# Kernel tuning notes

Hardware: AMD Instinct MI355X
Metric: run time of the kernel (lower is better)

The kernel has to match this reference:

```python
import jax, jax.numpy as jnp
import numpy as np

B, U, F = 32768, 256, 256  # batch, units, input features
LR = 0.01                  # inner_lr
EPS = 1e-3                 # TF LayerNormalization default epsilon


def _layer_norm(x, gamma, beta):
    m = jnp.mean(x, axis=-1, keepdims=True)
    v = jnp.var(x, axis=-1, keepdims=True)
    return (x - m) * jax.lax.rsqrt(v + EPS) * gamma + beta


def _enc(W1, b1, W2, b2, u):
    # mlp_2 inner encoder: Dense(4U, gelu-exact) -> Dense(U)
    return jax.nn.gelu(u @ W1 + b1, approximate=False) @ W2 + b2


def setup_inputs() -> dict:
    key = jax.random.key(0)
    ks = jax.random.split(key, 12)
    def w(k, shape):
        fan_in = shape[0]
        return jax.random.normal(k, shape, jnp.float32) / np.sqrt(fan_in)
    return {
        "x": jax.random.normal(ks[0], (B, F), jnp.float32),
        "h_prev": jax.random.normal(ks[1], (B, U), jnp.float32),
        "W_phi": w(ks[2], (F + U, U)), "b_phi": jnp.zeros((U,), jnp.float32),
        "W_psi": w(ks[3], (F + U, U)), "b_psi": jnp.zeros((U,), jnp.float32),
        "W1": w(ks[4], (U, 4 * U)), "b1": jnp.zeros((4 * U,), jnp.float32),
        "W2": w(ks[5], (4 * U, U)), "b2": jnp.zeros((U,), jnp.float32),
        "W_g": w(ks[6], (U, U)), "g_bias": jnp.zeros((U,), jnp.float32),
        "ln_gamma": jnp.ones((U,), jnp.float32), "ln_beta": jnp.zeros((U,), jnp.float32),
        "W_h": w(ks[7], (U, U)), "h_bias": jnp.zeros((U,), jnp.float32),
    }


def reference(x, h_prev, W_phi, b_phi, W_psi, b_psi, W1, b1, W2, b2,
              W_g, g_bias, ln_gamma, ln_beta, W_h, h_bias):
    z = jnp.concatenate([x, h_prev], axis=-1)          # [B, F+U]
    phi = z @ W_phi + b_phi                            # [B, U], also the inner target

    def inner_loss(params):
        W1_, b1_, W2_, b2_ = params
        r = _enc(W1_, b1_, W2_, b2_, phi) @ W_g + g_bias
        r = _layer_norm(r, ln_gamma, ln_beta)
        return jnp.mean(jnp.square(r - phi)), r

    params = (W1, b1, W2, b2)
    # inner_iterations = 1: one SGD step on the inner-encoder weights only
    (_, recon), grads = jax.value_and_grad(inner_loss, has_aux=True)(params)
    params = tuple(p - LR * g for p, g in zip(params, grads))

    psi = z @ W_psi + b_psi                            # [B, U]
    feat = _enc(*params, psi) + 0.1 * recon            # updated encoder on psi
    out = feat @ W_h + h_bias                          # new hidden / cell output
    return out
```

## Files before the change

kernel.cpp:

```cpp
#include <hip/hip_runtime.h>
#include <math.h>

#define B_N 32768
#define U_N 256
#define H_N 1024
#define LR_C 0.01f
#define EPS_C 1e-3f

typedef unsigned short ushort_t;
typedef unsigned int uint_t;
using frag8 = __attribute__((ext_vector_type(8))) short;
using f32x4 = __attribute__((ext_vector_type(4))) float;

__device__ __forceinline__ float erf_fast(float y) {
    float ay = fabsf(y);
    float t = __builtin_amdgcn_rcpf(fmaf(0.3275911f, ay, 1.0f));
    float p = fmaf(1.061405429f, t, -1.453152027f);
    p = fmaf(p, t, 1.421413741f);
    p = fmaf(p, t, -0.284496736f);
    p = fmaf(p, t, 0.254829592f);
    p = p * t;
    float e = __expf(-ay * ay);
    float r = fmaf(-p, e, 1.0f);
    return copysignf(r, y);
}
__device__ __forceinline__ float gelu_f(float x) {
    return 0.5f * x * (1.0f + erf_fast(x * 0.7071067811865475f));
}
__device__ __forceinline__ float dgelu_f(float x) {
    float c = 0.5f * (1.0f + erf_fast(x * 0.7071067811865475f));
    float p = 0.3989422804014327f * __expf(-0.5f * x * x);
    return fmaf(x, p, c);
}
__device__ __forceinline__ void splitf(float v, ushort_t& h, ushort_t& l) {
    uint_t u = __float_as_uint(v);
    h = (ushort_t)(u >> 16);
    float r = v - __uint_as_float(u & 0xFFFF0000u);
    uint_t ru = __float_as_uint(r);
    l = (ushort_t)((ru + 0x7FFFu + ((ru >> 16) & 1u)) >> 16);
}
__device__ __forceinline__ ushort_t cvt_rne(float v) {
    uint_t u = __float_as_uint(v);
    return (ushort_t)((u + 0x7FFFu + ((u >> 16) & 1u)) >> 16);
}
__device__ __forceinline__ float bf2f(ushort_t u) {
    return __uint_as_float((uint_t)u << 16);
}
__device__ __forceinline__ void unpack2(uint_t pa, uint_t pb, uint_t& hw, uint_t& lw) {
    hw = __builtin_amdgcn_perm(pb, pa, 0x07060302u);
    lw = __builtin_amdgcn_perm(pb, pa, 0x05040100u);
}

#define EPI_NONE 0
#define EPI_GELU 1
#define EPI_ADDS 3

#define BEP_P   0
#define BEP_PT  1
#define BEP_A1  2
#define BEP_DAT 3

template<int ACONCAT, int APACK, int EPI, int OPACK>
__global__ __launch_bounds__(256)
void mgemm_k(const float* A, const float* A2, const uint_t* __restrict__ AP,
             const ushort_t* __restrict__ BTh, const ushort_t* __restrict__ BTl,
             const float* __restrict__ bias, const ushort_t* __restrict__ Xr,
             float* C, uint_t* Cp,
             int M, int N, int K)
{
    __shared__ ushort_t Ah[128 * 40], Al[128 * 40];
    __shared__ ushort_t Bh[128 * 40], Bl[128 * 40];
    const int tid = threadIdx.x;
    const int m0 = blockIdx.x * 128, n0 = blockIdx.y * 128;
    const int lane = tid & 63, w = tid >> 6;
    const int wm = (w & 1) * 64, wn = (w >> 1) * 64;
    const int fr = lane & 15, fq = lane >> 4;
    const int sr = tid >> 1;
    const int sk = (tid & 1) * 16;

    f32x4 acc[4][4];
    #pragma unroll
    for (int i = 0; i < 4; i++)
        #pragma unroll
        for (int j = 0; j < 4; j++) acc[i][j] = (f32x4){0.f, 0.f, 0.f, 0.f};

    for (int k0 = 0; k0 < K; k0 += 32) {
        if (APACK) {
            const uint_t* ap = AP + (size_t)(m0 + sr) * K + k0 + sk;
            uint4 p0 = *(const uint4*)(ap);
            uint4 p1 = *(const uint4*)(ap + 4);
            uint4 p2 = *(const uint4*)(ap + 8);
            uint4 p3 = *(const uint4*)(ap + 12);
            uint4 h0, h1, l0, l1;
            unpack2(p0.x, p0.y, h0.x, l0.x); unpack2(p0.z, p0.w, h0.y, l0.y);
            unpack2(p1.x, p1.y, h0.z, l0.z); unpack2(p1.z, p1.w, h0.w, l0.w);
            unpack2(p2.x, p2.y, h1.x, l1.x); unpack2(p2.z, p2.w, h1.y, l1.y);
            unpack2(p3.x, p3.y, h1.z, l1.z); unpack2(p3.z, p3.w, h1.w, l1.w);
            *(uint4*)&Ah[sr * 40 + sk]     = h0;
            *(uint4*)&Ah[sr * 40 + sk + 8] = h1;
            *(uint4*)&Al[sr * 40 + sk]     = l0;
            *(uint4*)&Al[sr * 40 + sk + 8] = l1;
        } else {
            #pragma unroll
            for (int g = 0; g < 2; g++) {
                uint4 qh, qa;
                uint_t ph[4], pl[4];
                #pragma unroll
                for (int c = 0; c < 2; c++) {
                    const int ak = k0 + sk + g * 8 + c * 4;
                    const float* ap;
                    if (ACONCAT) ap = (ak < 256) ? (A + (size_t)(m0 + sr) * 256 + ak)
                                                 : (A2 + (size_t)(m0 + sr) * 256 + (ak - 256));
                    else         ap = A + (size_t)(m0 + sr) * K + ak;
                    float4 v = *(const float4*)ap;
                    ushort_t h0,h1,h2,h3,l0,l1,l2,l3;
                    splitf(v.x,h0,l0); splitf(v.y,h1,l1); splitf(v.z,h2,l2); splitf(v.w,h3,l3);
                    ph[c*2]   = (uint_t)h0 | ((uint_t)h1 << 16);
                    ph[c*2+1] = (uint_t)h2 | ((uint_t)h3 << 16);
                    pl[c*2]   = (uint_t)l0 | ((uint_t)l1 << 16);
                    pl[c*2+1] = (uint_t)l2 | ((uint_t)l3 << 16);
                }
                qh.x = ph[0]; qh.y = ph[1]; qh.z = ph[2]; qh.w = ph[3];
                qa.x = pl[0]; qa.y = pl[1]; qa.z = pl[2]; qa.w = pl[3];
                *(uint4*)&Ah[sr * 40 + sk + g * 8] = qh;
                *(uint4*)&Al[sr * 40 + sk + g * 8] = qa;
            }
        }
        {
            const size_t bo = (size_t)(n0 + sr) * K + k0 + sk;
            *(uint4*)&Bh[sr * 40 + sk]     = *(const uint4*)&BTh[bo];
            *(uint4*)&Bh[sr * 40 + sk + 8] = *(const uint4*)&BTh[bo + 8];
            *(uint4*)&Bl[sr * 40 + sk]     = *(const uint4*)&BTl[bo];
            *(uint4*)&Bl[sr * 40 + sk + 8] = *(const uint4*)&BTl[bo + 8];
        }
        __syncthreads();

        frag8 afh[4], afl[4], bfh[4], bfl[4];
        #pragma unroll
        for (int i = 0; i < 4; i++) {
            const int ar = wm + i * 16 + fr;
            afh[i] = *(frag8*)&Ah[ar * 40 + fq * 8];
            afl[i] = *(frag8*)&Al[ar * 40 + fq * 8];
        }
        #pragma unroll
        for (int j = 0; j < 4; j++) {
            const int br = wn + j * 16 + fr;
            bfh[j] = *(frag8*)&Bh[br * 40 + fq * 8];
            bfl[j] = *(frag8*)&Bl[br * 40 + fq * 8];
        }
        #pragma unroll
        for (int i = 0; i < 4; i++)
            #pragma unroll
            for (int j = 0; j < 4; j++) {
                acc[i][j] = __builtin_amdgcn_mfma_f32_16x16x32_bf16(afh[i], bfh[j], acc[i][j], 0, 0, 0);
                acc[i][j] = __builtin_amdgcn_mfma_f32_16x16x32_bf16(afh[i], bfl[j], acc[i][j], 0, 0, 0);
                acc[i][j] = __builtin_amdgcn_mfma_f32_16x16x32_bf16(afl[i], bfh[j], acc[i][j], 0, 0, 0);
            }
        __syncthreads();
    }

    float bv[4] = {0.f, 0.f, 0.f, 0.f};
    if (bias != nullptr)
        #pragma unroll
        for (int j = 0; j < 4; j++) bv[j] = bias[n0 + wn + j * 16 + fr];
    #pragma unroll
    for (int i = 0; i < 4; i++)
        #pragma unroll
        for (int j = 0; j < 4; j++) {
            const int col = n0 + wn + j * 16 + fr;
            #pragma unroll
            for (int r = 0; r < 4; r++) {
                const int row = m0 + wm + i * 16 + fq * 4 + r;
                const size_t off = (size_t)row * N + col;
                float c = acc[i][j][r] + bv[j];
                if (EPI == EPI_GELU)      c = gelu_f(c);
                else if (EPI == EPI_ADDS) c = c + 0.1f * bf2f(Xr[off]);
                if (OPACK) {
                    ushort_t h, l;
                    splitf(c, h, l);
                    Cp[off] = ((uint_t)h << 16) | (uint_t)l;
                } else {
                    C[off] = c;
                }
            }
        }
}

template<int ACONCAT, int BEP>
__global__ __launch_bounds__(256)
void bgemm_k(const void* Av, const float* A2f, const ushort_t* __restrict__ BTh,
             const float* __restrict__ bias, const ushort_t* __restrict__ GpIn,
             ushort_t* Crm, ushort_t* Cct, ushort_t* GpOut,
             int M, int N, int K)
{
    __shared__ ushort_t Ah[128 * 40];
    __shared__ ushort_t Bh[128 * 40];
    const int tid = threadIdx.x;
    const int m0 = blockIdx.x * 128, n0 = blockIdx.y * 128;
    const int lane = tid & 63, w = tid >> 6;
    const int wm = (w & 1) * 64, wn = (w >> 1) * 64;
    const int fr = lane & 15, fq = lane >> 4;
    const int sr = tid >> 1;
    const int sk = (tid & 1) * 16;

    f32x4 acc[4][4];
    #pragma unroll
    for (int i = 0; i < 4; i++)
        #pragma unroll
        for (int j = 0; j < 4; j++) acc[i][j] = (f32x4){0.f, 0.f, 0.f, 0.f};

    for (int k0 = 0; k0 < K; k0 += 32) {
        if (ACONCAT) {
            const float* A = (const float*)Av;
            #pragma unroll
            for (int g = 0; g < 2; g++) {
                uint_t ph[4];
                #pragma unroll
                for (int c = 0; c < 2; c++) {
                    const int ak = k0 + sk + g * 8 + c * 4;
                    const float* ap = (ak < 256) ? (A + (size_t)(m0 + sr) * 256 + ak)
                                                 : (A2f + (size_t)(m0 + sr) * 256 + (ak - 256));
                    float4 v = *(const float4*)ap;
                    ph[c*2]   = (uint_t)cvt_rne(v.x) | ((uint_t)cvt_rne(v.y) << 16);
                    ph[c*2+1] = (uint_t)cvt_rne(v.z) | ((uint_t)cvt_rne(v.w) << 16);
                }
                uint4 q; q.x = ph[0]; q.y = ph[1]; q.z = ph[2]; q.w = ph[3];
                *(uint4*)&Ah[sr * 40 + sk + g * 8] = q;
            }
        } else {
            const ushort_t* A = (const ushort_t*)Av;
            const size_t ao = (size_t)(m0 + sr) * K + k0 + sk;
            *(uint4*)&Ah[sr * 40 + sk]     = *(const uint4*)&A[ao];
            *(uint4*)&Ah[sr * 40 + sk + 8] = *(const uint4*)&A[ao + 8];
        }
        {
            const size_t bo = (size_t)(n0 + sr) * K + k0 + sk;
            *(uint4*)&Bh[sr * 40 + sk]     = *(const uint4*)&BTh[bo];
            *(uint4*)&Bh[sr * 40 + sk + 8] = *(const uint4*)&BTh[bo + 8];
        }
        __syncthreads();

        frag8 af[4], bf[4];
        #pragma unroll
        for (int i = 0; i < 4; i++) af[i] = *(frag8*)&Ah[(wm + i * 16 + fr) * 40 + fq * 8];
        #pragma unroll
        for (int j = 0; j < 4; j++) bf[j] = *(frag8*)&Bh[(wn + j * 16 + fr) * 40 + fq * 8];
        #pragma unroll
        for (int i = 0; i < 4; i++)
            #pragma unroll
            for (int j = 0; j < 4; j++)
                acc[i][j] = __builtin_amdgcn_mfma_f32_16x16x32_bf16(af[i], bf[j], acc[i][j], 0, 0, 0);
        __syncthreads();
    }

    float bv[4] = {0.f, 0.f, 0.f, 0.f};
    if (bias != nullptr)
        #pragma unroll
        for (int j = 0; j < 4; j++) bv[j] = bias[n0 + wn + j * 16 + fr];
    #pragma unroll
    for (int i = 0; i < 4; i++)
        #pragma unroll
        for (int j = 0; j < 4; j++) {
            const int col = n0 + wn + j * 16 + fr;
            const int rowb = m0 + wm + i * 16 + fq * 4;
            float v[4];
            #pragma unroll
            for (int r = 0; r < 4; r++) v[r] = acc[i][j][r] + bv[j];
            if (BEP == BEP_A1) {
                ushort_t gc[4];
                #pragma unroll
                for (int r = 0; r < 4; r++) {
                    float g = gelu_f(v[r]);
                    gc[r] = cvt_rne(g);
                    Crm[(size_t)(rowb + r) * N + col] = gc[r];
                    GpOut[(size_t)(rowb + r) * N + col] = cvt_rne(dgelu_f(v[r]));
                }
                uint_t p0 = (uint_t)gc[0] | ((uint_t)gc[1] << 16);
                uint_t p1 = (uint_t)gc[2] | ((uint_t)gc[3] << 16);
                *(uint2*)&Cct[(size_t)col * M + rowb] = (uint2){p0, p1};
            } else if (BEP == BEP_DAT) {
                ushort_t dc[4];
                #pragma unroll
                for (int r = 0; r < 4; r++)
                    dc[r] = cvt_rne(v[r] * bf2f(GpIn[(size_t)(rowb + r) * N + col]));
                uint_t p0 = (uint_t)dc[0] | ((uint_t)dc[1] << 16);
                uint_t p1 = (uint_t)dc[2] | ((uint_t)dc[3] << 16);
                *(uint2*)&Cct[(size_t)col * M + rowb] = (uint2){p0, p1};
            } else {
                ushort_t cc[4];
                #pragma unroll
                for (int r = 0; r < 4; r++) {
                    cc[r] = cvt_rne(v[r]);
                    Crm[(size_t)(rowb + r) * N + col] = cc[r];
                }
                if (BEP == BEP_PT) {
                    uint_t p0 = (uint_t)cc[0] | ((uint_t)cc[1] << 16);
                    uint_t p1 = (uint_t)cc[2] | ((uint_t)cc[3] << 16);
                    *(uint2*)&Cct[(size_t)col * M + rowb] = (uint2){p0, p1};
                }
            }
        }
}

__global__ __launch_bounds__(256)
void wgrad_k(const ushort_t* __restrict__ AT, const ushort_t* __restrict__ BTt,
             float* C, int M, int N, int KA, int kofsA, int KB, int kofsB, int KC)
{
    __shared__ ushort_t Ah[128 * 40];
    __shared__ ushort_t Bh[128 * 40];
    const int tid = threadIdx.x;
    const int m0 = blockIdx.x * 128, n0 = blockIdx.y * 128;
    const int kbA = kofsA + blockIdx.z * KC;
    const int kbB = kofsB + blockIdx.z * KC;
    const int lane = tid & 63, w = tid >> 6;
    const int wm = (w & 1) * 64, wn = (w >> 1) * 64;
    const int fr = lane & 15, fq = lane >> 4;
    const int sr = tid >> 1;
    const int sk = (tid & 1) * 16;

    f32x4 acc[4][4];
    #pragma unroll
    for (int i = 0; i < 4; i++)
        #pragma unroll
        for (int j = 0; j < 4; j++) acc[i][j] = (f32x4){0.f, 0.f, 0.f, 0.f};

    for (int k0 = 0; k0 < KC; k0 += 32) {
        const size_t ao = (size_t)(m0 + sr) * KA + kbA + k0 + sk;
        *(uint4*)&Ah[sr * 40 + sk]     = *(const uint4*)&AT[ao];
        *(uint4*)&Ah[sr * 40 + sk + 8] = *(const uint4*)&AT[ao + 8];
        const size_t bo = (size_t)(n0 + sr) * KB + kbB + k0 + sk;
        *(uint4*)&Bh[sr * 40 + sk]     = *(const uint4*)&BTt[bo];
        *(uint4*)&Bh[sr * 40 + sk + 8] = *(const uint4*)&BTt[bo + 8];
        __syncthreads();

        frag8 af[4], bf[4];
        #pragma unroll
        for (int i = 0; i < 4; i++) af[i] = *(frag8*)&Ah[(wm + i * 16 + fr) * 40 + fq * 8];
        #pragma unroll
        for (int j = 0; j < 4; j++) bf[j] = *(frag8*)&Bh[(wn + j * 16 + fr) * 40 + fq * 8];
        #pragma unroll
        for (int i = 0; i < 4; i++)
            #pragma unroll
            for (int j = 0; j < 4; j++)
                acc[i][j] = __builtin_amdgcn_mfma_f32_16x16x32_bf16(af[i], bf[j], acc[i][j], 0, 0, 0);
        __syncthreads();
    }
    #pragma unroll
    for (int i = 0; i < 4; i++)
        #pragma unroll
        for (int j = 0; j < 4; j++) {
            const int col = n0 + wn + j * 16 + fr;
            #pragma unroll
            for (int r = 0; r < 4; r++) {
                const int row = m0 + wm + i * 16 + fq * 4 + r;
                atomicAdd(&C[(size_t)row * N + col], acc[i][j][r]);
            }
        }
}

__global__ __launch_bounds__(256)
void colsumT_k(const ushort_t* __restrict__ T, float* db, int LD, int cols)
{
    const int n = blockIdx.x * 4 + (threadIdx.x >> 6);
    const int lane = threadIdx.x & 63;
    const ushort_t* row = T + (size_t)n * LD;
    float s = 0.f;
    for (int c = lane * 8; c < cols; c += 512) {
        uint4 q = *(const uint4*)&row[c];
        uint_t u[4] = {q.x, q.y, q.z, q.w};
        #pragma unroll
        for (int t = 0; t < 4; t++) {
            s += bf2f((ushort_t)(u[t] & 0xFFFF));
            s += bf2f((ushort_t)(u[t] >> 16));
        }
    }
    #pragma unroll
    for (int o = 32; o > 0; o >>= 1) s += __shfl_xor(s, o);
    if (lane == 0) atomicAdd(&db[n], s);
}

__global__ __launch_bounds__(256)
void ln_bf_k(const ushort_t* r0, const ushort_t* __restrict__ phi,
             const float* __restrict__ gamma, const float* __restrict__ beta,
             ushort_t* recon, ushort_t* dr0)
{
    const int lane = threadIdx.x & 63;
    const int wv = threadIdx.x >> 6;
    const int row = blockIdx.x * 4 + wv;
    const size_t base = (size_t)row * U_N + (lane << 2);

    uint2 xu = *(const uint2*)(r0 + base);
    uint2 pu = *(const uint2*)(phi + base);
    float xs[4] = { bf2f((ushort_t)(xu.x & 0xFFFF)), bf2f((ushort_t)(xu.x >> 16)),
                    bf2f((ushort_t)(xu.y & 0xFFFF)), bf2f((ushort_t)(xu.y >> 16)) };
    float ps[4] = { bf2f((ushort_t)(pu.x & 0xFFFF)), bf2f((ushort_t)(pu.x >> 16)),
                    bf2f((ushort_t)(pu.y & 0xFFFF)), bf2f((ushort_t)(pu.y >> 16)) };
    float s = xs[0] + xs[1] + xs[2] + xs[3];
    float sq = xs[0]*xs[0] + xs[1]*xs[1] + xs[2]*xs[2] + xs[3]*xs[3];
    #pragma unroll
    for (int o = 32; o > 0; o >>= 1) { s += __shfl_xor(s, o); sq += __shfl_xor(sq, o); }
    const float m   = s * (1.0f / U_N);
    const float var = sq * (1.0f / U_N) - m * m;
    const float inv = rsqrtf(var + EPS_C);

    float4 gv = *(const float4*)(gamma + (lane << 2));
    float4 bvv = *(const float4*)(beta + (lane << 2));
    float gs[4] = {gv.x, gv.y, gv.z, gv.w};
    float bs[4] = {bvv.x, bvv.y, bvv.z, bvv.w};
    float rh[4], dh[4], rc[4];
    float s1 = 0.f, s2 = 0.f;
    const float gscale = 2.0f / ((float)B_N * (float)U_N);
    #pragma unroll
    for (int j = 0; j < 4; j++) {
        rh[j] = (xs[j] - m) * inv;
        rc[j] = rh[j] * gs[j] + bs[j];
        float g2 = gscale * (rc[j] - ps[j]);
        dh[j] = g2 * gs[j];
        s1 += dh[j];
        s2 += dh[j] * rh[j];
    }
    #pragma unroll
    for (int o = 32; o > 0; o >>= 1) { s1 += __shfl_xor(s1, o); s2 += __shfl_xor(s2, o); }
    const float mu1 = s1 * (1.0f / U_N);
    const float mu2 = s2 * (1.0f / U_N);
    ushort_t oc[4], dc[4];
    #pragma unroll
    for (int j = 0; j < 4; j++) {
        oc[j] = cvt_rne(rc[j]);
        dc[j] = cvt_rne(inv * (dh[j] - mu1 - rh[j] * mu2));
    }
    *(uint2*)(recon + base) = (uint2){ (uint_t)oc[0] | ((uint_t)oc[1] << 16),
                                       (uint_t)oc[2] | ((uint_t)oc[3] << 16) };
    *(uint2*)(dr0 + base)   = (uint2){ (uint_t)dc[0] | ((uint_t)dc[1] << 16),
                                       (uint_t)dc[2] | ((uint_t)dc[3] << 16) };
}

template<int HASL>
__global__ __launch_bounds__(256)
void tsplit_k(const float* __restrict__ W, ushort_t* __restrict__ Th,
              ushort_t* __restrict__ Tl, int R, int C)
{
    __shared__ float t[64][65];
    const int tid = threadIdx.x;
    const int R0 = blockIdx.x * 64, C0 = blockIdx.y * 64;
    const int c = tid & 63, rb = (tid >> 6) * 16;
    for (int i = 0; i < 16; i++)
        t[rb + i][c] = W[(size_t)(R0 + rb + i) * C + C0 + c];
    __syncthreads();
    const int orr = tid & 63, ob = (tid >> 6) * 16;
    for (int i = 0; i < 16; i++) {
        const int oc = ob + i;
        ushort_t h, l;
        splitf(t[orr][oc], h, l);
        Th[(size_t)(C0 + oc) * R + R0 + orr] = h;
        if (HASL) Tl[(size_t)(C0 + oc) * R + R0 + orr] = l;
    }
}

__global__ __launch_bounds__(256)
void tupd_k(const float* __restrict__ W, const float* __restrict__ dW,
            ushort_t* __restrict__ Th, ushort_t* __restrict__ Tl, int R, int C)
{
    __shared__ float t[64][65];
    const int tid = threadIdx.x;
    const int R0 = blockIdx.x * 64, C0 = blockIdx.y * 64;
    const int c = tid & 63, rb = (tid >> 6) * 16;
    for (int i = 0; i < 16; i++) {
        const size_t o = (size_t)(R0 + rb + i) * C + C0 + c;
        t[rb + i][c] = W[o] - LR_C * dW[o];
    }
    __syncthreads();
    const int orr = tid & 63, ob = (tid >> 6) * 16;
    for (int i = 0; i < 16; i++) {
        const int oc = ob + i;
        ushort_t h, l;
        splitf(t[orr][oc], h, l);
        Th[(size_t)(C0 + oc) * R + R0 + orr] = h;
        Tl[(size_t)(C0 + oc) * R + R0 + orr] = l;
    }
}

__global__ __launch_bounds__(256)
void scvt_k(const float* __restrict__ W, ushort_t* __restrict__ Th, int n4)
{
    const int i = blockIdx.x * 256 + threadIdx.x;
    if (i >= n4) return;
    float4 v = *(const float4*)(W + (size_t)i * 4);
    uint2 ph;
    ph.x = (uint_t)cvt_rne(v.x) | ((uint_t)cvt_rne(v.y) << 16);
    ph.y = (uint_t)cvt_rne(v.z) | ((uint_t)cvt_rne(v.w) << 16);
    *(uint2*)&Th[(size_t)i * 4] = ph;
}

__global__ __launch_bounds__(256)
void bupd_k(const float* __restrict__ b1, const float* __restrict__ db1,
            const float* __restrict__ b2, const float* __restrict__ db2,
            float* __restrict__ b1u, float* __restrict__ b2u)
{
    const int i = blockIdx.x * 256 + threadIdx.x;
    if (i < H_N) b1u[i] = b1[i] - LR_C * db1[i];
    else if (i < H_N + U_N) b2u[i - H_N] = b2[i - H_N] - LR_C * db2[i - H_N];
}

extern "C" void kernel_launch(void* const* d_in, const int* in_sizes, int n_in,
                              void* d_out, int out_size, void* d_ws, size_t ws_size,
                              hipStream_t stream)
{
    const float* x      = (const float*)d_in[0];
    const float* h_prev = (const float*)d_in[1];
    const float* W_phi  = (const float*)d_in[2];
    const float* b_phi  = (const float*)d_in[3];
    const float* W_psi  = (const float*)d_in[4];
    const float* b_psi  = (const float*)d_in[5];
    const float* W1     = (const float*)d_in[6];
    const float* b1     = (const float*)d_in[7];
    const float* W2     = (const float*)d_in[8];
    const float* b2     = (const float*)d_in[9];
    const float* W_g    = (const float*)d_in[10];
    const float* g_bias = (const float*)d_in[11];
    const float* gamma  = (const float*)d_in[12];
    const float* beta   = (const float*)d_in[13];
    const float* W_h    = (const float*)d_in[14];
    const float* h_bias = (const float*)d_in[15];
    float* out = (float*)d_out;

    const size_t BU = (size_t)B_N * U_N;
    const size_t UH = (size_t)U_N * H_N;

    float* ws  = (float*)d_ws;
    float* dW1 = ws;
    float* db1 = dW1 + UH;
    float* dW2 = db1 + H_N;
    float* db2 = dW2 + UH;
    float* b1u = db2 + U_N;
    float* b2u = b1u + H_N;
    ushort_t* us = (ushort_t*)(((uintptr_t)(b2u + U_N) + 15) & ~(uintptr_t)15);
    ushort_t* WphiT_h = us;
    ushort_t* WpsiT_h = WphiT_h + 131072;     ushort_t* WpsiT_l = WpsiT_h + 131072;
    ushort_t* W1T_h   = WpsiT_l + 131072;
    ushort_t* W2T_h   = W1T_h + 262144;
    ushort_t* W2s_h   = W2T_h + 262144;
    ushort_t* Wgs_h   = W2s_h + 262144;
    ushort_t* WgT_h   = Wgs_h + 65536;
    ushort_t* W1uT_h  = WgT_h + 65536;        ushort_t* W1uT_l = W1uT_h + 262144;
    ushort_t* W2uT_h  = W1uT_l + 262144;      ushort_t* W2uT_l = W2uT_h + 262144;
    ushort_t* WhT_h   = W2uT_l + 262144;      ushort_t* WhT_l  = WhT_h + 65536;
    ushort_t* phi_bf  = WhT_l + 65536;
    ushort_t* phiT_bf = phi_bf + BU;
    ushort_t* recon_bf= phiT_bf + BU;
    ushort_t* chunk0  = recon_bf + BU;
    const size_t P_bytes = (size_t)((char*)chunk0 - (char*)d_ws);

    int GA = 2;
    while (GA < 256 && P_bytes + (size_t)(B_N / GA) * 10240 + (1 << 20) > ws_size) GA *= 2;
    size_t region = (size_t)(B_N / GA) * 10240;
    int GC = 1;
    while (GC < 256) {
        size_t cC = (size_t)(B_N / GC) * 6144;
        size_t r = cC > region ? cC : region;
        if (P_bytes + r + (1 << 20) <= ws_size) { region = r; break; }
        GC *= 2;
    }
    const int BcA = B_N / GA;
    const int BcC = B_N / GC;
    const int KC = (BcA >= 8192) ? 512 : ((BcA >= 1024) ? BcA / 16 : BcA);
    const int Z  = BcA / KC;

    ushort_t* g1  = chunk0;
    ushort_t* gp  = g1  + (size_t)BcA * H_N;
    ushort_t* g1T = gp  + (size_t)BcA * H_N;
    ushort_t* daT = g1T + (size_t)BcA * H_N;
    ushort_t* e_b = daT + (size_t)BcA * H_N;
    ushort_t* r0b = e_b + (size_t)BcA * U_N;
    ushort_t* deb = r0b + (size_t)BcA * U_N;
    ushort_t* deT = deb + (size_t)BcA * U_N;
    uint_t* psi_p  = (uint_t*)chunk0;
    uint_t* h2_p   = psi_p + (size_t)BcC * U_N;
    uint_t* feat_p = h2_p  + (size_t)BcC * H_N;

    hipMemsetAsync(dW1, 0, (2 * UH + H_N + U_N) * sizeof(float), stream);

    dim3 blk(256);
    tsplit_k<0><<<dim3(8, 4),  blk, 0, stream>>>(W_phi, WphiT_h, nullptr, 512, 256);
    tsplit_k<1><<<dim3(8, 4),  blk, 0, stream>>>(W_psi, WpsiT_h, WpsiT_l, 512, 256);
    tsplit_k<0><<<dim3(4, 16), blk, 0, stream>>>(W1, W1T_h, nullptr, 256, 1024);
    tsplit_k<0><<<dim3(16, 4), blk, 0, stream>>>(W2, W2T_h, nullptr, 1024, 256);
    tsplit_k<0><<<dim3(4, 4),  blk, 0, stream>>>(W_g, WgT_h, nullptr, 256, 256);
    tsplit_k<1><<<dim3(4, 4),  blk, 0, stream>>>(W_h, WhT_h, WhT_l, 256, 256);
    scvt_k<<<dim3(256), blk, 0, stream>>>(W2, W2s_h, 65536);
    scvt_k<<<dim3(64),  blk, 0, stream>>>(W_g, Wgs_h, 16384);

    bgemm_k<1, BEP_PT><<<dim3(B_N / 128, 2), blk, 0, stream>>>(
        x, h_prev, WphiT_h, b_phi, nullptr, phi_bf, phiT_bf, nullptr, B_N, U_N, 512);

    for (int c = 0; c < GA; c++) {
        const size_t off = (size_t)c * BcA;
        const ushort_t* phic = phi_bf + off * U_N;
        bgemm_k<0, BEP_A1><<<dim3(BcA / 128, 8), blk, 0, stream>>>(
            phic, nullptr, W1T_h, b1, nullptr, g1, g1T, gp, BcA, H_N, U_N);
        bgemm_k<0, BEP_P><<<dim3(BcA / 128, 2), blk, 0, stream>>>(
            g1, nullptr, W2T_h, b2, nullptr, e_b, nullptr, nullptr, BcA, U_N, H_N);
        bgemm_k<0, BEP_P><<<dim3(BcA / 128, 2), blk, 0, stream>>>(
            e_b, nullptr, WgT_h, g_bias, nullptr, r0b, nullptr, nullptr, BcA, U_N, U_N);
        ln_bf_k<<<dim3(BcA / 4), blk, 0, stream>>>(r0b, phic, gamma, beta,
                                                   recon_bf + off * U_N, r0b);
        bgemm_k<0, BEP_PT><<<dim3(BcA / 128, 2), blk, 0, stream>>>(
            r0b, nullptr, Wgs_h, nullptr, nullptr, deb, deT, nullptr, BcA, U_N, U_N);
        bgemm_k<0, BEP_DAT><<<dim3(BcA / 128, 8), blk, 0, stream>>>(
            deb, nullptr, W2s_h, nullptr, gp, nullptr, daT, nullptr, BcA, H_N, U_N);
        wgrad_k<<<dim3(8, 2, Z), blk, 0, stream>>>(g1T, deT, dW2, H_N, U_N,
                                                   BcA, 0, BcA, 0, KC);
        colsumT_k<<<dim3(U_N / 4), blk, 0, stream>>>(deT, db2, BcA, BcA);
        wgrad_k<<<dim3(2, 8, Z), blk, 0, stream>>>(phiT_bf, daT, dW1, U_N, H_N,
                                                   B_N, (int)off, BcA, 0, KC);
        colsumT_k<<<dim3(H_N / 4), blk, 0, stream>>>(daT, db1, BcA, BcA);
    }

    bupd_k<<<dim3(5), blk, 0, stream>>>(b1, db1, b2, db2, b1u, b2u);
    tupd_k<<<dim3(4, 16), blk, 0, stream>>>(W1, dW1, W1uT_h, W1uT_l, 256, 1024);
    tupd_k<<<dim3(16, 4), blk, 0, stream>>>(W2, dW2, W2uT_h, W2uT_l, 1024, 256);

    for (int c = 0; c < GC; c++) {
        const size_t off = (size_t)c * BcC;
        mgemm_k<1, 0, EPI_NONE, 1><<<dim3(BcC / 128, 2), blk, 0, stream>>>(
            x + off * 256, h_prev + off * U_N, nullptr,
            WpsiT_h, WpsiT_l, b_psi, nullptr,
            nullptr, psi_p, BcC, U_N, 512);
        mgemm_k<0, 1, EPI_GELU, 1><<<dim3(BcC / 128, 8), blk, 0, stream>>>(
            nullptr, nullptr, psi_p,
            W1uT_h, W1uT_l, b1u, nullptr,
            nullptr, h2_p, BcC, H_N, U_N);
        mgemm_k<0, 1, EPI_ADDS, 1><<<dim3(BcC / 128, 2), blk, 0, stream>>>(
            nullptr, nullptr, h2_p,
            W2uT_h, W2uT_l, b2u, recon_bf + off * U_N,
            nullptr, feat_p, BcC, U_N, H_N);
        mgemm_k<0, 1, EPI_NONE, 0><<<dim3(BcC / 128, 2), blk, 0, stream>>>(
            nullptr, nullptr, feat_p,
            WhT_h, WhT_l, h_bias, nullptr,
            out + off * U_N, nullptr, BcC, U_N, U_N);
    }
}
```

Before: 876.7 us.

## Double-buffer LDS tiles with register prefetch and swap grid axes for N-major order

All three GEMM kernels now prefetch the next K-tile from global memory into registers while the MFMA loop runs on the current tile. The prefetched tile is then written into a second LDS buffer, so only one barrier is needed per iteration and load latency is hidden behind compute. The launch grids are also transposed so the N tiles vary fastest, letting neighbouring blocks share the same A rows in cache. The cost is double the LDS (80 KB dynamic for the split kernel) and more registers, which can lower occupancy.

```diff
diff --git a/kernel.cpp b/kernel.cpp
--- a/kernel.cpp
+++ b/kernel.cpp
@@ -68,10 +68,13 @@
              float* C, uint_t* Cp,
              int M, int N, int K)
 {
-    __shared__ ushort_t Ah[128 * 40], Al[128 * 40];
-    __shared__ ushort_t Bh[128 * 40], Bl[128 * 40];
+    extern __shared__ ushort_t smem[];
+    ushort_t* AhS = smem;
+    ushort_t* AlS = smem + 10240;
+    ushort_t* BhS = smem + 20480;
+    ushort_t* BlS = smem + 30720;
     const int tid = threadIdx.x;
-    const int m0 = blockIdx.x * 128, n0 = blockIdx.y * 128;
+    const int m0 = blockIdx.y * 128, n0 = blockIdx.x * 128;
     const int lane = tid & 63, w = tid >> 6;
     const int wm = (w & 1) * 64, wn = (w >> 1) * 64;
     const int fr = lane & 15, fq = lane >> 4;
@@ -84,57 +87,84 @@
         #pragma unroll
         for (int j = 0; j < 4; j++) acc[i][j] = (f32x4){0.f, 0.f, 0.f, 0.f};
 
-    for (int k0 = 0; k0 < K; k0 += 32) {
+    uint4 rA[4];
+    float4 rF[4];
+    uint4 rB[4];
+
+    auto load_tile = [&](int k0) {
         if (APACK) {
             const uint_t* ap = AP + (size_t)(m0 + sr) * K + k0 + sk;
-            uint4 p0 = *(const uint4*)(ap);
-            uint4 p1 = *(const uint4*)(ap + 4);
-            uint4 p2 = *(const uint4*)(ap + 8);
-            uint4 p3 = *(const uint4*)(ap + 12);
+            rA[0] = *(const uint4*)(ap);
+            rA[1] = *(const uint4*)(ap + 4);
+            rA[2] = *(const uint4*)(ap + 8);
+            rA[3] = *(const uint4*)(ap + 12);
+        } else {
+            #pragma unroll
+            for (int g = 0; g < 4; g++) {
+                const int ak = k0 + sk + g * 4;
+                const float* ap;
+                if (ACONCAT) ap = (ak < 256) ? (A + (size_t)(m0 + sr) * 256 + ak)
+                                             : (A2 + (size_t)(m0 + sr) * 256 + (ak - 256));
+                else         ap = A + (size_t)(m0 + sr) * K + ak;
+                rF[g] = *(const float4*)ap;
+            }
+        }
+        const size_t bo = (size_t)(n0 + sr) * K + k0 + sk;
+        rB[0] = *(const uint4*)&BTh[bo];
+        rB[1] = *(const uint4*)&BTh[bo + 8];
+        rB[2] = *(const uint4*)&BTl[bo];
+        rB[3] = *(const uint4*)&BTl[bo + 8];
+    };
+    auto store_tile = [&](int buf) {
+        ushort_t* Ah = AhS + buf * 5120;
+        ushort_t* Al = AlS + buf * 5120;
+        ushort_t* Bh = BhS + buf * 5120;
+        ushort_t* Bl = BlS + buf * 5120;
+        if (APACK) {
             uint4 h0, h1, l0, l1;
-            unpack2(p0.x, p0.y, h0.x, l0.x); unpack2(p0.z, p0.w, h0.y, l0.y);
-            unpack2(p1.x, p1.y, h0.z, l0.z); unpack2(p1.z, p1.w, h0.w, l0.w);
-            unpack2(p2.x, p2.y, h1.x, l1.x); unpack2(p2.z, p2.w, h1.y, l1.y);
-            unpack2(p3.x, p3.y, h1.z, l1.z); unpack2(p3.z, p3.w, h1.w, l1.w);
+            unpack2(rA[0].x, rA[0].y, h0.x, l0.x); unpack2(rA[0].z, rA[0].w, h0.y, l0.y);
+            unpack2(rA[1].x, rA[1].y, h0.z, l0.z); unpack2(rA[1].z, rA[1].w, h0.w, l0.w);
+            unpack2(rA[2].x, rA[2].y, h1.x, l1.x); unpack2(rA[2].z, rA[2].w, h1.y, l1.y);
+            unpack2(rA[3].x, rA[3].y, h1.z, l1.z); unpack2(rA[3].z, rA[3].w, h1.w, l1.w);
             *(uint4*)&Ah[sr * 40 + sk]     = h0;
             *(uint4*)&Ah[sr * 40 + sk + 8] = h1;
             *(uint4*)&Al[sr * 40 + sk]     = l0;
             *(uint4*)&Al[sr * 40 + sk + 8] = l1;
         } else {
-            #pragma unroll
-            for (int g = 0; g < 2; g++) {
-                uint4 qh, qa;
-                uint_t ph[4], pl[4];
-                #pragma unroll
-                for (int c = 0; c < 2; c++) {
-                    const int ak = k0 + sk + g * 8 + c * 4;
-                    const float* ap;
-                    if (ACONCAT) ap = (ak < 256) ? (A + (size_t)(m0 + sr) * 256 + ak)
-                                                 : (A2 + (size_t)(m0 + sr) * 256 + (ak - 256));
-                    else         ap = A + (size_t)(m0 + sr) * K + ak;
-                    float4 v = *(const float4*)ap;
-                    ushort_t h0,h1,h2,h3,l0,l1,l2,l3;
-                    splitf(v.x,h0,l0); splitf(v.y,h1,l1); splitf(v.z,h2,l2); splitf(v.w,h3,l3);
-                    ph[c*2]   = (uint_t)h0 | ((uint_t)h1 << 16);
-                    ph[c*2+1] = (uint_t)h2 | ((uint_t)h3 << 16);
-                    pl[c*2]   = (uint_t)l0 | ((uint_t)l1 << 16);
-                    pl[c*2+1] = (uint_t)l2 | ((uint_t)l3 << 16);
-                }
-                qh.x = ph[0]; qh.y = ph[1]; qh.z = ph[2]; qh.w = ph[3];
-                qa.x = pl[0]; qa.y = pl[1]; qa.z = pl[2]; qa.w = pl[3];
-                *(uint4*)&Ah[sr * 40 + sk + g * 8] = qh;
-                *(uint4*)&Al[sr * 40 + sk + g * 8] = qa;
+            uint_t ph[8], pl[8];
+            #pragma unroll
+            for (int g = 0; g < 4; g++) {
+                ushort_t h0, h1, h2, h3, l0, l1, l2, l3;
+                splitf(rF[g].x, h0, l0); splitf(rF[g].y, h1, l1);
+                splitf(rF[g].z, h2, l2); splitf(rF[g].w, h3, l3);
+                ph[g*2]   = (uint_t)h0 | ((uint_t)h1 << 16);
+                ph[g*2+1] = (uint_t)h2 | ((uint_t)h3 << 16);
+                pl[g*2]   = (uint_t)l0 | ((uint_t)l1 << 16);
+                pl[g*2+1] = (uint_t)l2 | ((uint_t)l3 << 16);
             }
-        }
-        {
-            const size_t bo = (size_t)(n0 + sr) * K + k0 + sk;
-            *(uint4*)&Bh[sr * 40 + sk]     = *(const uint4*)&BTh[bo];
-            *(uint4*)&Bh[sr * 40 + sk + 8] = *(const uint4*)&BTh[bo + 8];
-            *(uint4*)&Bl[sr * 40 + sk]     = *(const uint4*)&BTl[bo];
-            *(uint4*)&Bl[sr * 40 + sk + 8] = *(const uint4*)&BTl[bo + 8];
-        }
-        __syncthreads();
-
+            *(uint4*)&Ah[sr * 40 + sk]     = *(uint4*)&ph[0];
+            *(uint4*)&Ah[sr * 40 + sk + 8] = *(uint4*)&ph[4];
+            *(uint4*)&Al[sr * 40 + sk]     = *(uint4*)&pl[0];
+            *(uint4*)&Al[sr * 40 + sk + 8] = *(uint4*)&pl[4];
+        }
+        *(uint4*)&Bh[sr * 40 + sk]     = rB[0];
+        *(uint4*)&Bh[sr * 40 + sk + 8] = rB[1];
+        *(uint4*)&Bl[sr * 40 + sk]     = rB[2];
+        *(uint4*)&Bl[sr * 40 + sk + 8] = rB[3];
+    };
+
+    load_tile(0);
+    store_tile(0);
+    __syncthreads();
+    const int nk = K >> 5;
+    for (int t = 0; t < nk; t++) {
+        const int cur = t & 1;
+        if (t + 1 < nk) load_tile((t + 1) << 5);
+
+        const ushort_t* Ah = AhS + cur * 5120;
+        const ushort_t* Al = AlS + cur * 5120;
+        const ushort_t* Bh = BhS + cur * 5120;
+        const ushort_t* Bl = BlS + cur * 5120;
         frag8 afh[4], afl[4], bfh[4], bfl[4];
         #pragma unroll
         for (int i = 0; i < 4; i++) {
@@ -156,6 +186,7 @@
                 acc[i][j] = __builtin_amdgcn_mfma_f32_16x16x32_bf16(afh[i], bfl[j], acc[i][j], 0, 0, 0);
                 acc[i][j] = __builtin_amdgcn_mfma_f32_16x16x32_bf16(afl[i], bfh[j], acc[i][j], 0, 0, 0);
             }
+        if (t + 1 < nk) store_tile(cur ^ 1);
         __syncthreads();
     }
 
@@ -193,10 +224,10 @@
              ushort_t* Crm, ushort_t* Cct, ushort_t* GpOut,
              int M, int N, int K)
 {
-    __shared__ ushort_t Ah[128 * 40];
-    __shared__ ushort_t Bh[128 * 40];
+    __shared__ ushort_t AhS[2 * 5120];
+    __shared__ ushort_t BhS[2 * 5120];
     const int tid = threadIdx.x;
-    const int m0 = blockIdx.x * 128, n0 = blockIdx.y * 128;
+    const int m0 = blockIdx.y * 128, n0 = blockIdx.x * 128;
     const int lane = tid & 63, w = tid >> 6;
     const int wm = (w & 1) * 64, wn = (w >> 1) * 64;
     const int fr = lane & 15, fq = lane >> 4;
@@ -209,37 +240,60 @@
         #pragma unroll
         for (int j = 0; j < 4; j++) acc[i][j] = (f32x4){0.f, 0.f, 0.f, 0.f};
 
-    for (int k0 = 0; k0 < K; k0 += 32) {
+    float4 rF[4];
+    uint4 rA[2];
+    uint4 rB[2];
+
+    auto load_tile = [&](int k0) {
         if (ACONCAT) {
             const float* A = (const float*)Av;
             #pragma unroll
-            for (int g = 0; g < 2; g++) {
-                uint_t ph[4];
-                #pragma unroll
-                for (int c = 0; c < 2; c++) {
-                    const int ak = k0 + sk + g * 8 + c * 4;
-                    const float* ap = (ak < 256) ? (A + (size_t)(m0 + sr) * 256 + ak)
-                                                 : (A2f + (size_t)(m0 + sr) * 256 + (ak - 256));
-                    float4 v = *(const float4*)ap;
-                    ph[c*2]   = (uint_t)cvt_rne(v.x) | ((uint_t)cvt_rne(v.y) << 16);
-                    ph[c*2+1] = (uint_t)cvt_rne(v.z) | ((uint_t)cvt_rne(v.w) << 16);
-                }
-                uint4 q; q.x = ph[0]; q.y = ph[1]; q.z = ph[2]; q.w = ph[3];
-                *(uint4*)&Ah[sr * 40 + sk + g * 8] = q;
+            for (int g = 0; g < 4; g++) {
+                const int ak = k0 + sk + g * 4;
+                const float* ap = (ak < 256) ? (A + (size_t)(m0 + sr) * 256 + ak)
+                                             : (A2f + (size_t)(m0 + sr) * 256 + (ak - 256));
+                rF[g] = *(const float4*)ap;
             }
         } else {
             const ushort_t* A = (const ushort_t*)Av;
             const size_t ao = (size_t)(m0 + sr) * K + k0 + sk;
-            *(uint4*)&Ah[sr * 40 + sk]     = *(const uint4*)&A[ao];
-            *(uint4*)&Ah[sr * 40 + sk + 8] = *(const uint4*)&A[ao + 8];
-        }
-        {
-            const size_t bo = (size_t)(n0 + sr) * K + k0 + sk;
-            *(uint4*)&Bh[sr * 40 + sk]     = *(const uint4*)&BTh[bo];
-            *(uint4*)&Bh[sr * 40 + sk + 8] = *(const uint4*)&BTh[bo + 8];
-        }
-        __syncthreads();
-
+            rA[0] = *(const uint4*)&A[ao];
+            rA[1] = *(const uint4*)&A[ao + 8];
+        }
+        const size_t bo = (size_t)(n0 + sr) * K + k0 + sk;
+        rB[0] = *(const uint4*)&BTh[bo];
+        rB[1] = *(const uint4*)&BTh[bo + 8];
+    };
+    auto store_tile = [&](int buf) {
+        ushort_t* Ah = AhS + buf * 5120;
+        ushort_t* Bh = BhS + buf * 5120;
+        if (ACONCAT) {
+            uint_t ph[8];
+            #pragma unroll
+            for (int g = 0; g < 4; g++) {
+                ph[g*2]   = (uint_t)cvt_rne(rF[g].x) | ((uint_t)cvt_rne(rF[g].y) << 16);
+                ph[g*2+1] = (uint_t)cvt_rne(rF[g].z) | ((uint_t)cvt_rne(rF[g].w) << 16);
+            }
+            *(uint4*)&Ah[sr * 40 + sk]     = *(uint4*)&ph[0];
+            *(uint4*)&Ah[sr * 40 + sk + 8] = *(uint4*)&ph[4];
+        } else {
+            *(uint4*)&Ah[sr * 40 + sk]     = rA[0];
+            *(uint4*)&Ah[sr * 40 + sk + 8] = rA[1];
+        }
+        *(uint4*)&Bh[sr * 40 + sk]     = rB[0];
+        *(uint4*)&Bh[sr * 40 + sk + 8] = rB[1];
+    };
+
+    load_tile(0);
+    store_tile(0);
+    __syncthreads();
+    const int nk = K >> 5;
+    for (int t = 0; t < nk; t++) {
+        const int cur = t & 1;
+        if (t + 1 < nk) load_tile((t + 1) << 5);
+
+        const ushort_t* Ah = AhS + cur * 5120;
+        const ushort_t* Bh = BhS + cur * 5120;
         frag8 af[4], bf[4];
         #pragma unroll
         for (int i = 0; i < 4; i++) af[i] = *(frag8*)&Ah[(wm + i * 16 + fr) * 40 + fq * 8];
@@ -250,6 +304,7 @@
             #pragma unroll
             for (int j = 0; j < 4; j++)
                 acc[i][j] = __builtin_amdgcn_mfma_f32_16x16x32_bf16(af[i], bf[j], acc[i][j], 0, 0, 0);
+        if (t + 1 < nk) store_tile(cur ^ 1);
         __syncthreads();
     }
 
@@ -306,10 +361,10 @@
 void wgrad_k(const ushort_t* __restrict__ AT, const ushort_t* __restrict__ BTt,
              float* C, int M, int N, int KA, int kofsA, int KB, int kofsB, int KC)
 {
-    __shared__ ushort_t Ah[128 * 40];
-    __shared__ ushort_t Bh[128 * 40];
+    __shared__ ushort_t AhS[2 * 5120];
+    __shared__ ushort_t BhS[2 * 5120];
     const int tid = threadIdx.x;
-    const int m0 = blockIdx.x * 128, n0 = blockIdx.y * 128;
+    const int m0 = blockIdx.y * 128, n0 = blockIdx.x * 128;
     const int kbA = kofsA + blockIdx.z * KC;
     const int kbB = kofsB + blockIdx.z * KC;
     const int lane = tid & 63, w = tid >> 6;
@@ -324,15 +379,33 @@
         #pragma unroll
         for (int j = 0; j < 4; j++) acc[i][j] = (f32x4){0.f, 0.f, 0.f, 0.f};
 
-    for (int k0 = 0; k0 < KC; k0 += 32) {
+    uint4 rA[2], rB[2];
+    auto load_tile = [&](int k0) {
         const size_t ao = (size_t)(m0 + sr) * KA + kbA + k0 + sk;
-        *(uint4*)&Ah[sr * 40 + sk]     = *(const uint4*)&AT[ao];
-        *(uint4*)&Ah[sr * 40 + sk + 8] = *(const uint4*)&AT[ao + 8];
+        rA[0] = *(const uint4*)&AT[ao];
+        rA[1] = *(const uint4*)&AT[ao + 8];
         const size_t bo = (size_t)(n0 + sr) * KB + kbB + k0 + sk;
-        *(uint4*)&Bh[sr * 40 + sk]     = *(const uint4*)&BTt[bo];
-        *(uint4*)&Bh[sr * 40 + sk + 8] = *(const uint4*)&BTt[bo + 8];
-        __syncthreads();
-
+        rB[0] = *(const uint4*)&BTt[bo];
+        rB[1] = *(const uint4*)&BTt[bo + 8];
+    };
+    auto store_tile = [&](int buf) {
+        ushort_t* Ah = AhS + buf * 5120;
+        ushort_t* Bh = BhS + buf * 5120;
+        *(uint4*)&Ah[sr * 40 + sk]     = rA[0];
+        *(uint4*)&Ah[sr * 40 + sk + 8] = rA[1];
+        *(uint4*)&Bh[sr * 40 + sk]     = rB[0];
+        *(uint4*)&Bh[sr * 40 + sk + 8] = rB[1];
+    };
+
+    load_tile(0);
+    store_tile(0);
+    __syncthreads();
+    const int nk = KC >> 5;
+    for (int t = 0; t < nk; t++) {
+        const int cur = t & 1;
+        if (t + 1 < nk) load_tile((t + 1) << 5);
+        const ushort_t* Ah = AhS + cur * 5120;
+        const ushort_t* Bh = BhS + cur * 5120;
         frag8 af[4], bf[4];
         #pragma unroll
         for (int i = 0; i < 4; i++) af[i] = *(frag8*)&Ah[(wm + i * 16 + fr) * 40 + fq * 8];
@@ -343,6 +416,7 @@
             #pragma unroll
             for (int j = 0; j < 4; j++)
                 acc[i][j] = __builtin_amdgcn_mfma_f32_16x16x32_bf16(af[i], bf[j], acc[i][j], 0, 0, 0);
+        if (t + 1 < nk) store_tile(cur ^ 1);
         __syncthreads();
     }
     #pragma unroll
@@ -581,6 +655,7 @@
     hipMemsetAsync(dW1, 0, (2 * UH + H_N + U_N) * sizeof(float), stream);
 
     dim3 blk(256);
+    const int MLDS = 81920;
     tsplit_k<0><<<dim3(8, 4),  blk, 0, stream>>>(W_phi, WphiT_h, nullptr, 512, 256);
     tsplit_k<1><<<dim3(8, 4),  blk, 0, stream>>>(W_psi, WpsiT_h, WpsiT_l, 512, 256);
     tsplit_k<0><<<dim3(4, 16), blk, 0, stream>>>(W1, W1T_h, nullptr, 256, 1024);
@@ -590,28 +665,28 @@
     scvt_k<<<dim3(256), blk, 0, stream>>>(W2, W2s_h, 65536);
     scvt_k<<<dim3(64),  blk, 0, stream>>>(W_g, Wgs_h, 16384);
 
-    bgemm_k<1, BEP_PT><<<dim3(B_N / 128, 2), blk, 0, stream>>>(
+    bgemm_k<1, BEP_PT><<<dim3(2, B_N / 128), blk, 0, stream>>>(
         x, h_prev, WphiT_h, b_phi, nullptr, phi_bf, phiT_bf, nullptr, B_N, U_N, 512);
 
     for (int c = 0; c < GA; c++) {
         const size_t off = (size_t)c * BcA;
         const ushort_t* phic = phi_bf + off * U_N;
-        bgemm_k<0, BEP_A1><<<dim3(BcA / 128, 8), blk, 0, stream>>>(
+        bgemm_k<0, BEP_A1><<<dim3(8, BcA / 128), blk, 0, stream>>>(
             phic, nullptr, W1T_h, b1, nullptr, g1, g1T, gp, BcA, H_N, U_N);
-        bgemm_k<0, BEP_P><<<dim3(BcA / 128, 2), blk, 0, stream>>>(
+        bgemm_k<0, BEP_P><<<dim3(2, BcA / 128), blk, 0, stream>>>(
             g1, nullptr, W2T_h, b2, nullptr, e_b, nullptr, nullptr, BcA, U_N, H_N);
-        bgemm_k<0, BEP_P><<<dim3(BcA / 128, 2), blk, 0, stream>>>(
+        bgemm_k<0, BEP_P><<<dim3(2, BcA / 128), blk, 0, stream>>>(
             e_b, nullptr, WgT_h, g_bias, nullptr, r0b, nullptr, nullptr, BcA, U_N, U_N);
         ln_bf_k<<<dim3(BcA / 4), blk, 0, stream>>>(r0b, phic, gamma, beta,
                                                    recon_bf + off * U_N, r0b);
-        bgemm_k<0, BEP_PT><<<dim3(BcA / 128, 2), blk, 0, stream>>>(
+        bgemm_k<0, BEP_PT><<<dim3(2, BcA / 128), blk, 0, stream>>>(
             r0b, nullptr, Wgs_h, nullptr, nullptr, deb, deT, nullptr, BcA, U_N, U_N);
-        bgemm_k<0, BEP_DAT><<<dim3(BcA / 128, 8), blk, 0, stream>>>(
+        bgemm_k<0, BEP_DAT><<<dim3(8, BcA / 128), blk, 0, stream>>>(
             deb, nullptr, W2s_h, nullptr, gp, nullptr, daT, nullptr, BcA, H_N, U_N);
-        wgrad_k<<<dim3(8, 2, Z), blk, 0, stream>>>(g1T, deT, dW2, H_N, U_N,
+        wgrad_k<<<dim3(2, 8, Z), blk, 0, stream>>>(g1T, deT, dW2, H_N, U_N,
                                                    BcA, 0, BcA, 0, KC);
         colsumT_k<<<dim3(U_N / 4), blk, 0, stream>>>(deT, db2, BcA, BcA);
-        wgrad_k<<<dim3(2, 8, Z), blk, 0, stream>>>(phiT_bf, daT, dW1, U_N, H_N,
+        wgrad_k<<<dim3(8, 2, Z), blk, 0, stream>>>(phiT_bf, daT, dW1, U_N, H_N,
                                                    B_N, (int)off, BcA, 0, KC);
         colsumT_k<<<dim3(H_N / 4), blk, 0, stream>>>(daT, db1, BcA, BcA);
     }
@@ -622,19 +697,19 @@
 
     for (int c = 0; c < GC; c++) {
         const size_t off = (size_t)c * BcC;
-        mgemm_k<1, 0, EPI_NONE, 1><<<dim3(BcC / 128, 2), blk, 0, stream>>>(
+        mgemm_k<1, 0, EPI_NONE, 1><<<dim3(2, BcC / 128), blk, MLDS, stream>>>(
             x + off * 256, h_prev + off * U_N, nullptr,
             WpsiT_h, WpsiT_l, b_psi, nullptr,
             nullptr, psi_p, BcC, U_N, 512);
-        mgemm_k<0, 1, EPI_GELU, 1><<<dim3(BcC / 128, 8), blk, 0, stream>>>(
+        mgemm_k<0, 1, EPI_GELU, 1><<<dim3(8, BcC / 128), blk, MLDS, stream>>>(
             nullptr, nullptr, psi_p,
             W1uT_h, W1uT_l, b1u, nullptr,
             nullptr, h2_p, BcC, H_N, U_N);
-        mgemm_k<0, 1, EPI_ADDS, 1><<<dim3(BcC / 128, 2), blk, 0, stream>>>(
+        mgemm_k<0, 1, EPI_ADDS, 1><<<dim3(2, BcC / 128), blk, MLDS, stream>>>(
             nullptr, nullptr, h2_p,
             W2uT_h, W2uT_l, b2u, recon_bf + off * U_N,
             nullptr, feat_p, BcC, U_N, H_N);
-        mgemm_k<0, 1, EPI_NONE, 0><<<dim3(BcC / 128, 2), blk, 0, stream>>>(
+        mgemm_k<0, 1, EPI_NONE, 0><<<dim3(2, BcC / 128), blk, MLDS, stream>>>(
             nullptr, nullptr, feat_p,
             WhT_h, WhT_l, h_bias, nullptr,
             out + off * U_N, nullptr, BcC, U_N, U_N);
```

Result: slower. 1.379 ms (+57.3%).

## Load B tiles via direct global-to-LDS loads with pre-swizzled weight layout

Applied to the files above, without the earlier changes.

B operand tiles in both GEMM kernels are now fetched with global_load_lds 16-byte direct-to-LDS loads instead of passing through registers. Because that path cannot pad rows, the weight-prep kernels write a pre-swizzled XOR layout in global memory and the fragment reads apply the matching swizzle to avoid LDS bank conflicts. A fused gelu_pair also computes gelu and its derivative from one erf and exp evaluation in the forward epilogue. Every consumer of the transposed weights must agree on the swizzle, and scvt_k assumes a row width of 256.

```diff
diff --git a/kernel.cpp b/kernel.cpp
--- a/kernel.cpp
+++ b/kernel.cpp
@@ -32,6 +32,20 @@
     float p = 0.3989422804014327f * __expf(-0.5f * x * x);
     return fmaf(x, p, c);
 }
+__device__ __forceinline__ void gelu_pair(float x, float& g, float& d) {
+    float ay = fabsf(x) * 0.7071067811865475f;
+    float t = __builtin_amdgcn_rcpf(fmaf(0.3275911f, ay, 1.0f));
+    float p = fmaf(1.061405429f, t, -1.453152027f);
+    p = fmaf(p, t, 1.421413741f);
+    p = fmaf(p, t, -0.284496736f);
+    p = fmaf(p, t, 0.254829592f);
+    p = p * t;
+    float e = __expf(-ay * ay);
+    float er = copysignf(fmaf(-p, e, 1.0f), x);
+    float c = 0.5f * (1.0f + er);
+    g = x * c;
+    d = fmaf(x * 0.3989422804014327f, e, c);
+}
 __device__ __forceinline__ void splitf(float v, ushort_t& h, ushort_t& l) {
     uint_t u = __float_as_uint(v);
     h = (ushort_t)(u >> 16);
@@ -50,6 +64,15 @@
     hw = __builtin_amdgcn_perm(pb, pa, 0x07060302u);
     lw = __builtin_amdgcn_perm(pb, pa, 0x05040100u);
 }
+__device__ __forceinline__ size_t swz(int n, int k, int K) {
+    return (size_t)n * K +
+           (size_t)((k & ~31) | ((((k >> 3) & 3) ^ ((n >> 1) & 3)) << 3) | (k & 7));
+}
+__device__ __forceinline__ void gload16(const ushort_t* g, ushort_t* l) {
+    __builtin_amdgcn_global_load_lds(
+        (const __attribute__((address_space(1))) void*)g,
+        (__attribute__((address_space(3))) void*)l, 16, 0, 0);
+}
 
 #define EPI_NONE 0
 #define EPI_GELU 1
@@ -69,7 +92,7 @@
              int M, int N, int K)
 {
     __shared__ ushort_t Ah[128 * 40], Al[128 * 40];
-    __shared__ ushort_t Bh[128 * 40], Bl[128 * 40];
+    __shared__ ushort_t Bh[128 * 32], Bl[128 * 32];
     const int tid = threadIdx.x;
     const int m0 = blockIdx.x * 128, n0 = blockIdx.y * 128;
     const int lane = tid & 63, w = tid >> 6;
@@ -85,6 +108,14 @@
         for (int j = 0; j < 4; j++) acc[i][j] = (f32x4){0.f, 0.f, 0.f, 0.f};
 
     for (int k0 = 0; k0 < K; k0 += 32) {
+        {
+            const int r0w = w * 32;
+            const size_t so = (size_t)(n0 + r0w + (lane >> 2)) * K + k0 + ((lane & 3) << 3);
+            gload16(&BTh[so],                  &Bh[r0w * 32]);
+            gload16(&BTh[so + (size_t)16 * K], &Bh[(r0w + 16) * 32]);
+            gload16(&BTl[so],                  &Bl[r0w * 32]);
+            gload16(&BTl[so + (size_t)16 * K], &Bl[(r0w + 16) * 32]);
+        }
         if (APACK) {
             const uint_t* ap = AP + (size_t)(m0 + sr) * K + k0 + sk;
             uint4 p0 = *(const uint4*)(ap);
@@ -126,13 +157,6 @@
                 *(uint4*)&Al[sr * 40 + sk + g * 8] = qa;
             }
         }
-        {
-            const size_t bo = (size_t)(n0 + sr) * K + k0 + sk;
-            *(uint4*)&Bh[sr * 40 + sk]     = *(const uint4*)&BTh[bo];
-            *(uint4*)&Bh[sr * 40 + sk + 8] = *(const uint4*)&BTh[bo + 8];
-            *(uint4*)&Bl[sr * 40 + sk]     = *(const uint4*)&BTl[bo];
-            *(uint4*)&Bl[sr * 40 + sk + 8] = *(const uint4*)&BTl[bo + 8];
-        }
         __syncthreads();
 
         frag8 afh[4], afl[4], bfh[4], bfl[4];
@@ -145,8 +169,9 @@
         #pragma unroll
         for (int j = 0; j < 4; j++) {
             const int br = wn + j * 16 + fr;
-            bfh[j] = *(frag8*)&Bh[br * 40 + fq * 8];
-            bfl[j] = *(frag8*)&Bl[br * 40 + fq * 8];
+            const int bs = br * 32 + ((fq ^ ((br >> 1) & 3)) << 3);
+            bfh[j] = *(frag8*)&Bh[bs];
+            bfl[j] = *(frag8*)&Bl[bs];
         }
         #pragma unroll
         for (int i = 0; i < 4; i++)
@@ -194,7 +219,7 @@
              int M, int N, int K)
 {
     __shared__ ushort_t Ah[128 * 40];
-    __shared__ ushort_t Bh[128 * 40];
+    __shared__ ushort_t Bh[128 * 32];
     const int tid = threadIdx.x;
     const int m0 = blockIdx.x * 128, n0 = blockIdx.y * 128;
     const int lane = tid & 63, w = tid >> 6;
@@ -210,6 +235,12 @@
         for (int j = 0; j < 4; j++) acc[i][j] = (f32x4){0.f, 0.f, 0.f, 0.f};
 
     for (int k0 = 0; k0 < K; k0 += 32) {
+        {
+            const int r0w = w * 32;
+            const size_t so = (size_t)(n0 + r0w + (lane >> 2)) * K + k0 + ((lane & 3) << 3);
+            gload16(&BTh[so],                  &Bh[r0w * 32]);
+            gload16(&BTh[so + (size_t)16 * K], &Bh[(r0w + 16) * 32]);
+        }
         if (ACONCAT) {
             const float* A = (const float*)Av;
             #pragma unroll
@@ -233,18 +264,16 @@
             *(uint4*)&Ah[sr * 40 + sk]     = *(const uint4*)&A[ao];
             *(uint4*)&Ah[sr * 40 + sk + 8] = *(const uint4*)&A[ao + 8];
         }
-        {
-            const size_t bo = (size_t)(n0 + sr) * K + k0 + sk;
-            *(uint4*)&Bh[sr * 40 + sk]     = *(const uint4*)&BTh[bo];
-            *(uint4*)&Bh[sr * 40 + sk + 8] = *(const uint4*)&BTh[bo + 8];
-        }
         __syncthreads();
 
         frag8 af[4], bf[4];
         #pragma unroll
         for (int i = 0; i < 4; i++) af[i] = *(frag8*)&Ah[(wm + i * 16 + fr) * 40 + fq * 8];
         #pragma unroll
-        for (int j = 0; j < 4; j++) bf[j] = *(frag8*)&Bh[(wn + j * 16 + fr) * 40 + fq * 8];
+        for (int j = 0; j < 4; j++) {
+            const int br = wn + j * 16 + fr;
+            bf[j] = *(frag8*)&Bh[br * 32 + ((fq ^ ((br >> 1) & 3)) << 3)];
+        }
         #pragma unroll
         for (int i = 0; i < 4; i++)
             #pragma unroll
@@ -270,10 +299,11 @@
                 ushort_t gc[4];
                 #pragma unroll
                 for (int r = 0; r < 4; r++) {
-                    float g = gelu_f(v[r]);
+                    float g, d;
+                    gelu_pair(v[r], g, d);
                     gc[r] = cvt_rne(g);
                     Crm[(size_t)(rowb + r) * N + col] = gc[r];
-                    GpOut[(size_t)(rowb + r) * N + col] = cvt_rne(dgelu_f(v[r]));
+                    GpOut[(size_t)(rowb + r) * N + col] = cvt_rne(d);
                 }
                 uint_t p0 = (uint_t)gc[0] | ((uint_t)gc[1] << 16);
                 uint_t p1 = (uint_t)gc[2] | ((uint_t)gc[3] << 16);
@@ -452,8 +482,9 @@
         const int oc = ob + i;
         ushort_t h, l;
         splitf(t[orr][oc], h, l);
-        Th[(size_t)(C0 + oc) * R + R0 + orr] = h;
-        if (HASL) Tl[(size_t)(C0 + oc) * R + R0 + orr] = l;
+        const size_t d = swz(C0 + oc, R0 + orr, R);
+        Th[d] = h;
+        if (HASL) Tl[d] = l;
     }
 }
 
@@ -475,8 +506,9 @@
         const int oc = ob + i;
         ushort_t h, l;
         splitf(t[orr][oc], h, l);
-        Th[(size_t)(C0 + oc) * R + R0 + orr] = h;
-        Tl[(size_t)(C0 + oc) * R + R0 + orr] = l;
+        const size_t d = swz(C0 + oc, R0 + orr, R);
+        Th[d] = h;
+        Tl[d] = l;
     }
 }
 
@@ -486,10 +518,12 @@
     const int i = blockIdx.x * 256 + threadIdx.x;
     if (i >= n4) return;
     float4 v = *(const float4*)(W + (size_t)i * 4);
+    const int f = i * 4;
+    const int row = f >> 8, col = f & 255;
     uint2 ph;
     ph.x = (uint_t)cvt_rne(v.x) | ((uint_t)cvt_rne(v.y) << 16);
     ph.y = (uint_t)cvt_rne(v.z) | ((uint_t)cvt_rne(v.w) << 16);
-    *(uint2*)&Th[(size_t)i * 4] = ph;
+    *(uint2*)&Th[swz(row, col, 256)] = ph;
 }
 
 __global__ __launch_bounds__(256)
```

New measurement: 873.6 us. Within noise of the previous version (-0.3%).
